# Optimization experiments

Measured on AMD Instinct MI355X. Metric: run time of the kernel, lower is better.

The kernel has to match this reference:

```python
import jax, jax.numpy as jnp
import numpy as np

N, E, D, H = 100000, 200000, 384, 768
BN_EPS = 1e-5


def setup_inputs() -> dict:
    key = jax.random.key(0)
    ks = jax.random.split(key, 8)
    w = lambda k, sh: jax.random.normal(k, sh, jnp.float32) * 0.02
    return {
        "x": jax.random.normal(ks[0], (N, D), jnp.float32),
        "edge_attr": jax.random.normal(ks[1], (E, D), jnp.float32),
        "gamma": jnp.ones((D,), jnp.float32),
        "beta": jnp.zeros((D,), jnp.float32),
        "eps": jnp.zeros((), jnp.float32),          # GINE train_eps, init 0
        "W_edge": w(ks[2], (D, D)),
        "b_edge": jnp.zeros((D,), jnp.float32),
        "W1": w(ks[3], (D, H)),
        "b1": jnp.zeros((H,), jnp.float32),
        "W2": w(ks[4], (H, D)),
        "b2": jnp.zeros((D,), jnp.float32),
        "edge_index": jax.random.randint(ks[5], (2, E), 0, N, jnp.int32),
    }


def reference(x, edge_attr, gamma, beta, eps, W_edge, b_edge, W1, b1, W2, b2, edge_index):
    # BatchNorm1d over the node (batch) dimension, training statistics
    mu = jnp.mean(x, axis=0)
    var = jnp.var(x, axis=0)
    h = (x - mu) * jax.lax.rsqrt(var + BN_EPS) * gamma + beta  # [N, D]

    src, dst = edge_index[0], edge_index[1]  # j -> i (PyG source_to_target)
    # GINEConv message: relu(x_j + lin(edge_attr))
    msg = jax.nn.relu(h[src] + edge_attr @ W_edge + b_edge)     # [E, D]
    agg = jax.ops.segment_sum(msg, dst, num_segments=N)         # sum aggregation

    # nn((1+eps)*x_i + agg) where nn = Linear->GELU->Linear
    z = (1.0 + eps) * h + agg
    z = jax.nn.gelu(z @ W1 + b1, approximate=False) @ W2 + b2

    # residual + outer GELU activation (drop_path/dropout = identity at eval)
    return x + jax.nn.gelu(z, approximate=False)
```

## Files before the change

### kernel.cpp

```cpp
#include <hip/hip_runtime.h>
#include <hip/hip_bf16.h>

#define Df 384
#define Hf 768
#define SCAN_CH 4096

typedef __bf16 bf16x8 __attribute__((ext_vector_type(8)));
typedef float f32x4 __attribute__((ext_vector_type(4)));

struct __attribute__((aligned(4))) U12 { unsigned int x, y, z; };

__device__ inline unsigned short f2bf(float f) {
    __hip_bfloat16 h = __float2bfloat16(f);
    return __builtin_bit_cast(unsigned short, h);
}
__device__ inline float bf2f(unsigned short u) {
    unsigned int v = ((unsigned int)u) << 16;
    return __builtin_bit_cast(float, v);
}
__device__ inline float lobf(unsigned int v) { return bf2f((unsigned short)(v & 0xffff)); }
__device__ inline float hibf(unsigned int v) { return bf2f((unsigned short)(v >> 16)); }
__device__ inline unsigned int pk2(float a, float b) {
    return (unsigned int)f2bf(a) | ((unsigned int)f2bf(b) << 16);
}
__device__ inline float gelu_(float v) {
    return 0.5f * v * (1.0f + erff(v * 0.70710678118654752f));
}
__device__ inline void gload16(const void* g, void* l) {
    __builtin_amdgcn_global_load_lds(
        (const __attribute__((address_space(1))) unsigned int*)g,
        (__attribute__((address_space(3))) unsigned int*)l, 16, 0, 0);
}

__global__ void bn_stats(const float* __restrict__ x, float* __restrict__ stats, int N) {
    int t = threadIdx.x;
    int c4 = (t % 96) * 4;
    int rs = t / 96;
    float s0 = 0, s1 = 0, s2 = 0, s3 = 0, q0 = 0, q1 = 0, q2 = 0, q3 = 0;
    for (int r = blockIdx.x * 2 + rs; r < N; r += gridDim.x * 2) {
        float4 v = *(const float4*)(x + (size_t)r * Df + c4);
        s0 += v.x; s1 += v.y; s2 += v.z; s3 += v.w;
        q0 += v.x * v.x; q1 += v.y * v.y; q2 += v.z * v.z; q3 += v.w * v.w;
    }
    unsafeAtomicAdd(&stats[c4 + 0], s0);
    unsafeAtomicAdd(&stats[c4 + 1], s1);
    unsafeAtomicAdd(&stats[c4 + 2], s2);
    unsafeAtomicAdd(&stats[c4 + 3], s3);
    unsafeAtomicAdd(&stats[Df + c4 + 0], q0);
    unsafeAtomicAdd(&stats[Df + c4 + 1], q1);
    unsafeAtomicAdd(&stats[Df + c4 + 2], q2);
    unsafeAtomicAdd(&stats[Df + c4 + 3], q3);
}

__global__ void bn_finalize(const float* __restrict__ stats,
                            const float* __restrict__ gamma,
                            const float* __restrict__ beta,
                            float* __restrict__ coef, int N) {
    int c = threadIdx.x;
    float invN = 1.0f / (float)N;
    float mu = stats[c] * invN;
    float var = stats[Df + c] * invN - mu * mu;
    float rs = rsqrtf(var + 1e-5f);
    float a = gamma[c] * rs;
    coef[c] = a;
    coef[Df + c] = beta[c] - mu * a;
}

__global__ void h_kernel(const float* __restrict__ x, const float* __restrict__ coef,
                         unsigned short* __restrict__ hb, int tot8) {
    int i = blockIdx.x * 256 + threadIdx.x;
    if (i >= tot8) return;
    size_t base = (size_t)i * 8;
    int c = (int)(base % Df);
    float4 x0 = *(const float4*)(x + base);
    float4 x1 = *(const float4*)(x + base + 4);
    const float* a = coef + c;
    const float* b = coef + Df + c;
    uint4 o;
    o.x = pk2(x0.x * a[0] + b[0], x0.y * a[1] + b[1]);
    o.y = pk2(x0.z * a[2] + b[2], x0.w * a[3] + b[3]);
    o.z = pk2(x1.x * a[4] + b[4], x1.y * a[5] + b[5]);
    o.w = pk2(x1.z * a[6] + b[6], x1.w * a[7] + b[7]);
    *(uint4*)(hb + base) = o;
}

__global__ void wtrans(const float* __restrict__ Wsrc, unsigned short* __restrict__ Wdst,
                       int K, int Nc) {
    int idx = blockIdx.x * 256 + threadIdx.x;
    if (idx >= K * Nc) return;
    int k = idx / Nc, n = idx % Nc;
    Wdst[(size_t)n * K + k] = f2bf(Wsrc[idx]);
}

__global__ void degree_k(const int* __restrict__ dst, int* __restrict__ deg, int E) {
    int e = blockIdx.x * 256 + threadIdx.x;
    if (e < E) atomicAdd(&deg[dst[e]], 1);
}

__global__ void scan1(const int* __restrict__ deg, int* __restrict__ off,
                      int* __restrict__ sums, int N) {
    __shared__ int ts[256];
    int t = threadIdx.x;
    int base = blockIdx.x * SCAN_CH + t * 16;
    int v[16];
    int s = 0;
    for (int j = 0; j < 16; j++) {
        int idx = base + j;
        int d = (idx < N) ? deg[idx] : 0;
        v[j] = s;
        s += d;
    }
    ts[t] = s;
    __syncthreads();
    for (int o = 1; o < 256; o <<= 1) {
        int add = (t >= o) ? ts[t - o] : 0;
        __syncthreads();
        ts[t] += add;
        __syncthreads();
    }
    int pre = t ? ts[t - 1] : 0;
    for (int j = 0; j < 16; j++) {
        int idx = base + j;
        if (idx < N) off[idx] = pre + v[j];
    }
    if (t == 255) sums[blockIdx.x] = ts[255];
}

__global__ void scan2(int* __restrict__ sums, int nb) {
    int acc = 0;
    for (int b = 0; b < nb; b++) { int v = sums[b]; sums[b] = acc; acc += v; }
    sums[nb] = acc;
}

__global__ void scan3(int* __restrict__ off, const int* __restrict__ sums, int N, int nb) {
    int idx = blockIdx.x * 256 + threadIdx.x;
    if (idx < N) off[idx] += sums[idx / SCAN_CH];
    else if (idx == N) off[N] = sums[nb];
}

__global__ void fill_k(const int* __restrict__ dst, const int* __restrict__ src,
                       int* __restrict__ cursor, int* __restrict__ srcp,
                       int* __restrict__ pose, int E) {
    int e = blockIdx.x * 256 + threadIdx.x;
    if (e >= E) return;
    int pos = atomicAdd(&cursor[dst[e]], 1);
    srcp[pos] = src[e];
    pose[e] = pos;
}

__global__ __launch_bounds__(256) void aggregate(
    const unsigned short* __restrict__ msgl, const unsigned short* __restrict__ hb,
    const int* __restrict__ off, const int* __restrict__ srcp,
    const float* __restrict__ epsp,
    unsigned short* __restrict__ zb, int N) {
    int lane = threadIdx.x & 63;
    int wid = threadIdx.x >> 6;
    int nwaves = gridDim.x * 4;
    float s1p = 1.0f + epsp[0];
    int loff = lane * 6;
    for (int i = blockIdx.x * 4 + wid; i < N; i += nwaves) {
        int o0 = off[i], o1 = off[i + 1];
        float a0 = 0, a1 = 0, a2 = 0, a3 = 0, a4 = 0, a5 = 0;
        for (int p = o0; p < o1; ++p) {
            int s = srcp[p];
            U12 mv = *(const U12*)(msgl + (size_t)p * Df + loff);
            U12 hv = *(const U12*)(hb + (size_t)s * Df + loff);
            a0 += fmaxf(lobf(mv.x) + lobf(hv.x), 0.f);
            a1 += fmaxf(hibf(mv.x) + hibf(hv.x), 0.f);
            a2 += fmaxf(lobf(mv.y) + lobf(hv.y), 0.f);
            a3 += fmaxf(hibf(mv.y) + hibf(hv.y), 0.f);
            a4 += fmaxf(lobf(mv.z) + lobf(hv.z), 0.f);
            a5 += fmaxf(hibf(mv.z) + hibf(hv.z), 0.f);
        }
        U12 hv = *(const U12*)(hb + (size_t)i * Df + loff);
        U12 o;
        o.x = pk2(s1p * lobf(hv.x) + a0, s1p * hibf(hv.x) + a1);
        o.y = pk2(s1p * lobf(hv.y) + a2, s1p * hibf(hv.y) + a3);
        o.z = pk2(s1p * lobf(hv.z) + a4, s1p * hibf(hv.z) + a5);
        *(U12*)(zb + (size_t)i * Df + loff) = o;
    }
}

template <int EPI, bool ABF16>
__global__ __launch_bounds__(256) void gemm_fused(
    const void* __restrict__ Ap, const unsigned short* __restrict__ Bt,
    const float* __restrict__ bias, int M, int K,
    const int* __restrict__ pose,
    unsigned short* __restrict__ outb,
    const float* __restrict__ xres, float* __restrict__ outf, int ldo) {
    __shared__ __align__(16) unsigned short As[128 * 32];
    __shared__ __align__(16) unsigned short Bs[128 * 32];
    const int t = threadIdx.x;
    const int n0 = blockIdx.x * 128;
    const int m0 = blockIdx.y * 128;
    const int lane = t & 63;
    const int wid = t >> 6;
    const int wr = (wid >> 1) << 6;
    const int wc = (wid & 1) << 6;
    const int fr = lane & 15;
    const int kg = lane >> 4;
    const int crow = lane >> 2;
    const int cseg = lane & 3;
    const int sr = t >> 1;
    const int sh = (t & 1) << 4;

    f32x4 acc[4][4];
#pragma unroll
    for (int i = 0; i < 4; i++)
#pragma unroll
        for (int j = 0; j < 4; j++) acc[i][j] = (f32x4){0.f, 0.f, 0.f, 0.f};

    const bool arok = (m0 + sr) < M;
    const size_t arowoff = (size_t)(m0 + sr) * K;

    for (int k0 = 0; k0 < K; k0 += 32) {
        if (ABF16) {
            const unsigned short* Ab = (const unsigned short*)Ap;
#pragma unroll
            for (int c = 0; c < 2; c++) {
                const int row = wid * 32 + c * 16 + crow;
                if (m0 + row < M)
                    gload16(Ab + (size_t)(m0 + row) * K + k0 + cseg * 8,
                            &As[(wid * 32 + c * 16) * 32]);
            }
        } else {
            uint4 w0 = {0, 0, 0, 0}, w1 = {0, 0, 0, 0};
            if (arok) {
                const float4* p = (const float4*)((const float*)Ap + arowoff + k0 + sh);
                float4 f0 = p[0], f1 = p[1], f2 = p[2], f3 = p[3];
                w0.x = pk2(f0.x, f0.y); w0.y = pk2(f0.z, f0.w);
                w0.z = pk2(f1.x, f1.y); w0.w = pk2(f1.z, f1.w);
                w1.x = pk2(f2.x, f2.y); w1.y = pk2(f2.z, f2.w);
                w1.z = pk2(f3.x, f3.y); w1.w = pk2(f3.z, f3.w);
            }
            *(uint4*)&As[sr * 32 + sh] = w0;
            *(uint4*)&As[sr * 32 + sh + 8] = w1;
        }
#pragma unroll
        for (int c = 0; c < 2; c++) {
            const int row = wid * 32 + c * 16 + crow;
            gload16(Bt + (size_t)(n0 + row) * K + k0 + cseg * 8,
                    &Bs[(wid * 32 + c * 16) * 32]);
        }
        __syncthreads();
        bf16x8 a[4], b[4];
#pragma unroll
        for (int i = 0; i < 4; i++) a[i] = *(const bf16x8*)&As[(wr + i * 16 + fr) * 32 + kg * 8];
#pragma unroll
        for (int j = 0; j < 4; j++) b[j] = *(const bf16x8*)&Bs[(wc + j * 16 + fr) * 32 + kg * 8];
#pragma unroll
        for (int i = 0; i < 4; i++)
#pragma unroll
            for (int j = 0; j < 4; j++)
                acc[i][j] = __builtin_amdgcn_mfma_f32_16x16x32_bf16(a[i], b[j], acc[i][j], 0, 0, 0);
        __syncthreads();
    }

    const int kg4 = kg * 4;
#pragma unroll
    for (int i = 0; i < 4; i++) {
        const int rb = m0 + wr + i * 16 + kg4;
#pragma unroll
        for (int j = 0; j < 4; j++) {
            const int c = n0 + wc + j * 16 + fr;
#pragma unroll
            for (int r = 0; r < 4; r++) {
                const int row = rb + r;
                if (row < M) {
                    float v = acc[i][j][r] + bias[c];
                    if (EPI == 1) {
                        outb[(size_t)row * ldo + c] = f2bf(gelu_(v));
                    } else if (EPI == 2) {
                        size_t o = (size_t)row * ldo + c;
                        outf[o] = xres[o] + gelu_(v);
                    } else {
                        outb[(size_t)pose[row] * ldo + c] = f2bf(v);
                    }
                }
            }
        }
    }
}

extern "C" void kernel_launch(void* const* d_in, const int* in_sizes, int n_in,
                              void* d_out, int out_size, void* d_ws, size_t ws_size,
                              hipStream_t stream) {
    const float* x = (const float*)d_in[0];
    const float* ea = (const float*)d_in[1];
    const float* gamma = (const float*)d_in[2];
    const float* beta = (const float*)d_in[3];
    const float* epsp = (const float*)d_in[4];
    const float* W_edge = (const float*)d_in[5];
    const float* b_edge = (const float*)d_in[6];
    const float* W1 = (const float*)d_in[7];
    const float* b1 = (const float*)d_in[8];
    const float* W2 = (const float*)d_in[9];
    const float* b2 = (const float*)d_in[10];
    const int* eidx = (const int*)d_in[11];
    float* out = (float*)d_out;
    const int N = in_sizes[0] / Df;
    const int E = in_sizes[1] / Df;
    const int* esrc = eidx;
    const int* edst = eidx + E;

    char* w = (char*)d_ws;
    size_t off_ = 0;
    auto alloc = [&](size_t bytes) { char* p = w + off_; off_ += (bytes + 255) & ~(size_t)255; return p; };
    float* stats = (float*)alloc(2 * Df * sizeof(float));
    float* coef = (float*)alloc(2 * Df * sizeof(float));
    unsigned short* hb = (unsigned short*)alloc((size_t)N * Df * 2);
    unsigned short* zb = (unsigned short*)alloc((size_t)N * Df * 2);
    unsigned short* tb = (unsigned short*)alloc((size_t)N * Hf * 2);
    unsigned short* WeT = (unsigned short*)alloc((size_t)Df * Df * 2);
    unsigned short* W1T = (unsigned short*)alloc((size_t)Df * Hf * 2);
    unsigned short* W2T = (unsigned short*)alloc((size_t)Hf * Df * 2);
    int* deg = (int*)alloc((size_t)(N + 1) * 4);
    int* offs = (int*)alloc((size_t)(N + 1) * 4);
    int* srcp = (int*)alloc((size_t)E * 4);
    int* pose = (int*)alloc((size_t)E * 4);
    int* sums = (int*)alloc(64 * 4);
    size_t msgl_bytes = (size_t)E * Df * 2;
    unsigned short* msgl;
    if (off_ + msgl_bytes <= ws_size) msgl = (unsigned short*)alloc(msgl_bytes);
    else msgl = (unsigned short*)d_out;
    (void)n_in; (void)out_size;

    hipMemsetAsync(stats, 0, 2 * Df * sizeof(float), stream);
    hipMemsetAsync(deg, 0, (size_t)N * 4, stream);

    bn_stats<<<1024, 192, 0, stream>>>(x, stats, N);
    bn_finalize<<<1, Df, 0, stream>>>(stats, gamma, beta, coef, N);
    int tot8 = N * Df / 8;
    h_kernel<<<(tot8 + 255) / 256, 256, 0, stream>>>(x, coef, hb, tot8);

    wtrans<<<(Df * Df + 255) / 256, 256, 0, stream>>>(W_edge, WeT, Df, Df);
    wtrans<<<(Df * Hf + 255) / 256, 256, 0, stream>>>(W1, W1T, Df, Hf);
    wtrans<<<(Hf * Df + 255) / 256, 256, 0, stream>>>(W2, W2T, Hf, Df);

    int nb = (N + SCAN_CH - 1) / SCAN_CH;
    degree_k<<<(E + 255) / 256, 256, 0, stream>>>(edst, deg, E);
    scan1<<<nb, 256, 0, stream>>>(deg, offs, sums, N);
    scan2<<<1, 1, 0, stream>>>(sums, nb);
    scan3<<<(N + 256) / 256, 256, 0, stream>>>(offs, sums, N, nb);
    hipMemcpyAsync(deg, offs, (size_t)N * 4, hipMemcpyDeviceToDevice, stream);
    fill_k<<<(E + 255) / 256, 256, 0, stream>>>(edst, esrc, deg, srcp, pose, E);

    dim3 ge(Df / 128, (E + 127) / 128);
    gemm_fused<3, false><<<ge, 256, 0, stream>>>(ea, WeT, b_edge, E, Df,
                                                 pose, msgl, nullptr, nullptr, Df);

    aggregate<<<2048, 256, 0, stream>>>(msgl, hb, offs, srcp, epsp, zb, N);

    dim3 g1(Hf / 128, (N + 127) / 128);
    gemm_fused<1, true><<<g1, 256, 0, stream>>>(zb, W1T, b1, N, Df,
                                                nullptr, tb, nullptr, nullptr, Hf);
    dim3 g2(Df / 128, (N + 127) / 128);
    gemm_fused<2, true><<<g2, 256, 0, stream>>>(tb, W2T, b2, N, Hf,
                                                nullptr, nullptr, x, out, Df);
}
```

Before: 1.114 ms.

## Double-buffer GEMM LDS tiles and remap workgroups across XCDs

The GEMM kernel now double-buffers its A and B shared-memory tiles, so the global loads for the next K tile are issued before the MFMAs on the current tile. This removes one barrier per iteration and lets memory latency overlap with compute. Launches switch to a 1D grid whose block ids are remapped so consecutive tiles, which share A rows, land on the same XCD for better L2 reuse. The cost is twice the LDS per block, which may lower occupancy, plus more registers held across the loop for the fp32 A prefetch.

```diff
diff --git a/kernel.cpp b/kernel.cpp
--- a/kernel.cpp
+++ b/kernel.cpp
@@ -184,15 +184,22 @@
 template <int EPI, bool ABF16>
 __global__ __launch_bounds__(256) void gemm_fused(
     const void* __restrict__ Ap, const unsigned short* __restrict__ Bt,
-    const float* __restrict__ bias, int M, int K,
+    const float* __restrict__ bias, int M, int K, int ncols,
     const int* __restrict__ pose,
     unsigned short* __restrict__ outb,
     const float* __restrict__ xres, float* __restrict__ outf, int ldo) {
-    __shared__ __align__(16) unsigned short As[128 * 32];
-    __shared__ __align__(16) unsigned short Bs[128 * 32];
+    __shared__ __align__(16) unsigned short As[2][128 * 32];
+    __shared__ __align__(16) unsigned short Bs[2][128 * 32];
     const int t = threadIdx.x;
-    const int n0 = blockIdx.x * 128;
-    const int m0 = blockIdx.y * 128;
+    const int nwg = gridDim.x;
+    const int orig = blockIdx.x;
+    const int xcd = orig & 7;
+    const int q = nwg >> 3, r = nwg & 7;
+    const int wgid = (xcd < r ? xcd * (q + 1) : r * (q + 1) + (xcd - r) * q) + (orig >> 3);
+    const int pp = wgid / ncols;
+    const int m0 = pp * 128;
+    const int n0 = (wgid - pp * ncols) * 128;
+
     const int lane = t & 63;
     const int wid = t >> 6;
     const int wr = (wid >> 1) << 6;
@@ -212,48 +219,81 @@
 
     const bool arok = (m0 + sr) < M;
     const size_t arowoff = (size_t)(m0 + sr) * K;
-
-    for (int k0 = 0; k0 < K; k0 += 32) {
-        if (ABF16) {
-            const unsigned short* Ab = (const unsigned short*)Ap;
-#pragma unroll
-            for (int c = 0; c < 2; c++) {
-                const int row = wid * 32 + c * 16 + crow;
-                if (m0 + row < M)
-                    gload16(Ab + (size_t)(m0 + row) * K + k0 + cseg * 8,
-                            &As[(wid * 32 + c * 16) * 32]);
+    const int NT = K >> 5;
+
+    auto stageB = [&](int buf, int k0) {
+#pragma unroll
+        for (int h = 0; h < 2; h++) {
+            const int rbase = wid * 32 + h * 16;
+            gload16(Bt + (size_t)(n0 + rbase + crow) * K + k0 + cseg * 8,
+                    &Bs[buf][rbase * 32]);
+        }
+    };
+    auto stageA16 = [&](int buf, int k0) {
+        const unsigned short* Ab = (const unsigned short*)Ap;
+#pragma unroll
+        for (int h = 0; h < 2; h++) {
+            const int rbase = wid * 32 + h * 16;
+            if (m0 + rbase + crow < M)
+                gload16(Ab + (size_t)(m0 + rbase + crow) * K + k0 + cseg * 8,
+                        &As[buf][rbase * 32]);
+        }
+    };
+
+    if (ABF16) {
+        stageA16(0, 0);
+    } else if (arok) {
+        const float4* p = (const float4*)((const float*)Ap + arowoff + sh);
+        float4 f0 = p[0], f1 = p[1], f2 = p[2], f3 = p[3];
+        uint4 w0, w1;
+        w0.x = pk2(f0.x, f0.y); w0.y = pk2(f0.z, f0.w);
+        w0.z = pk2(f1.x, f1.y); w0.w = pk2(f1.z, f1.w);
+        w1.x = pk2(f2.x, f2.y); w1.y = pk2(f2.z, f2.w);
+        w1.z = pk2(f3.x, f3.y); w1.w = pk2(f3.z, f3.w);
+        *(uint4*)&As[0][sr * 32 + sh] = w0;
+        *(uint4*)&As[0][sr * 32 + sh + 8] = w1;
+    }
+    stageB(0, 0);
+    __syncthreads();
+
+    int cur = 0;
+    for (int kt = 0; kt < NT; ++kt) {
+        const int nxt = cur ^ 1;
+        const bool more = (kt + 1) < NT;
+        float4 f0, f1, f2, f3;
+        if (more) {
+            const int k0n = (kt + 1) * 32;
+            if (ABF16) {
+                stageA16(nxt, k0n);
+            } else if (arok) {
+                const float4* p = (const float4*)((const float*)Ap + arowoff + k0n + sh);
+                f0 = p[0]; f1 = p[1]; f2 = p[2]; f3 = p[3];
             }
-        } else {
-            uint4 w0 = {0, 0, 0, 0}, w1 = {0, 0, 0, 0};
-            if (arok) {
-                const float4* p = (const float4*)((const float*)Ap + arowoff + k0 + sh);
-                float4 f0 = p[0], f1 = p[1], f2 = p[2], f3 = p[3];
-                w0.x = pk2(f0.x, f0.y); w0.y = pk2(f0.z, f0.w);
-                w0.z = pk2(f1.x, f1.y); w0.w = pk2(f1.z, f1.w);
-                w1.x = pk2(f2.x, f2.y); w1.y = pk2(f2.z, f2.w);
-                w1.z = pk2(f3.x, f3.y); w1.w = pk2(f3.z, f3.w);
-            }
-            *(uint4*)&As[sr * 32 + sh] = w0;
-            *(uint4*)&As[sr * 32 + sh + 8] = w1;
-        }
-#pragma unroll
-        for (int c = 0; c < 2; c++) {
-            const int row = wid * 32 + c * 16 + crow;
-            gload16(Bt + (size_t)(n0 + row) * K + k0 + cseg * 8,
-                    &Bs[(wid * 32 + c * 16) * 32]);
-        }
-        __syncthreads();
+            stageB(nxt, k0n);
+        }
+
         bf16x8 a[4], b[4];
 #pragma unroll
-        for (int i = 0; i < 4; i++) a[i] = *(const bf16x8*)&As[(wr + i * 16 + fr) * 32 + kg * 8];
-#pragma unroll
-        for (int j = 0; j < 4; j++) b[j] = *(const bf16x8*)&Bs[(wc + j * 16 + fr) * 32 + kg * 8];
+        for (int i = 0; i < 4; i++) a[i] = *(const bf16x8*)&As[cur][(wr + i * 16 + fr) * 32 + kg * 8];
+#pragma unroll
+        for (int j = 0; j < 4; j++) b[j] = *(const bf16x8*)&Bs[cur][(wc + j * 16 + fr) * 32 + kg * 8];
 #pragma unroll
         for (int i = 0; i < 4; i++)
 #pragma unroll
             for (int j = 0; j < 4; j++)
                 acc[i][j] = __builtin_amdgcn_mfma_f32_16x16x32_bf16(a[i], b[j], acc[i][j], 0, 0, 0);
+
+        if (!ABF16 && more && arok) {
+            uint4 w0, w1;
+            w0.x = pk2(f0.x, f0.y); w0.y = pk2(f0.z, f0.w);
+            w0.z = pk2(f1.x, f1.y); w0.w = pk2(f1.z, f1.w);
+            w1.x = pk2(f2.x, f2.y); w1.y = pk2(f2.z, f2.w);
+            w1.z = pk2(f3.x, f3.y); w1.w = pk2(f3.z, f3.w);
+            *(uint4*)&As[nxt][sr * 32 + sh] = w0;
+            *(uint4*)&As[nxt][sr * 32 + sh + 8] = w1;
+        }
         __syncthreads();
+        cur = nxt;
     }
 
     const int kg4 = kg * 4;
@@ -345,16 +385,15 @@
     hipMemcpyAsync(deg, offs, (size_t)N * 4, hipMemcpyDeviceToDevice, stream);
     fill_k<<<(E + 255) / 256, 256, 0, stream>>>(edst, esrc, deg, srcp, pose, E);
 
-    dim3 ge(Df / 128, (E + 127) / 128);
-    gemm_fused<3, false><<<ge, 256, 0, stream>>>(ea, WeT, b_edge, E, Df,
-                                                 pose, msgl, nullptr, nullptr, Df);
+    int ep = (E + 127) / 128;
+    gemm_fused<3, false><<<dim3(ep * (Df / 128)), 256, 0, stream>>>(
+        ea, WeT, b_edge, E, Df, Df / 128, pose, msgl, nullptr, nullptr, Df);
 
     aggregate<<<2048, 256, 0, stream>>>(msgl, hb, offs, srcp, epsp, zb, N);
 
-    dim3 g1(Hf / 128, (N + 127) / 128);
-    gemm_fused<1, true><<<g1, 256, 0, stream>>>(zb, W1T, b1, N, Df,
-                                                nullptr, tb, nullptr, nullptr, Hf);
-    dim3 g2(Df / 128, (N + 127) / 128);
-    gemm_fused<2, true><<<g2, 256, 0, stream>>>(tb, W2T, b2, N, Hf,
-                                                nullptr, nullptr, x, out, Df);
-}
+    int np = (N + 127) / 128;
+    gemm_fused<1, true><<<dim3(np * (Hf / 128)), 256, 0, stream>>>(
+        zb, W1T, b1, N, Df, Hf / 128, nullptr, tb, nullptr, nullptr, Hf);
+    gemm_fused<2, true><<<dim3(np * (Df / 128)), 256, 0, stream>>>(
+        tb, W2T, b2, N, Hf, Df / 128, nullptr, nullptr, x, out, Df);
+}
```

New measurement: 1.085 ms. -2.6%, faster.

## Restructure GEMMs with 256x64 tiles, register-prefetched A and chunk-staged B

Applied to the files above, without the earlier changes.

Replaces the 128x128 LDS-tiled GEMM with a 256x64 tile kernel. Each wave streams its A rows straight from global memory into registers with a multi-stage prefetch, while B (the weights) is staged into LDS in large K chunks with an XOR swizzle. This cuts per-K-step barriers and LDS traffic for A. Workgroup IDs are remapped across XCDs for cache locality, and launch bounds request 3 waves per SIMD. The costs are higher register pressure and uncoalesced direct global reads for A fragments.

```diff
diff --git a/kernel.cpp b/kernel.cpp
--- a/kernel.cpp
+++ b/kernel.cpp
@@ -181,28 +181,38 @@
     }
 }
 
-template <int EPI, bool ABF16>
-__global__ __launch_bounds__(256) void gemm_fused(
+template <int NTK, int EPI, bool ABF16>
+__global__ __launch_bounds__(256, 3) void gemm2(
     const void* __restrict__ Ap, const unsigned short* __restrict__ Bt,
-    const float* __restrict__ bias, int M, int K,
+    const float* __restrict__ bias, int M, int ncols,
     const int* __restrict__ pose,
     unsigned short* __restrict__ outb,
     const float* __restrict__ xres, float* __restrict__ outf, int ldo) {
-    __shared__ __align__(16) unsigned short As[128 * 32];
-    __shared__ __align__(16) unsigned short Bs[128 * 32];
+    constexpr int K = NTK * 32;
+    constexpr int NCH = (NTK + 11) / 12;
+    constexpr int CKT = NTK / NCH;
+    constexpr int D = ABF16 ? 3 : 2;
+    constexpr int PW = ABF16 ? 4 : 8;
+    __shared__ __align__(16) unsigned short Bs[CKT * 64 * 32];
+
     const int t = threadIdx.x;
-    const int n0 = blockIdx.x * 128;
-    const int m0 = blockIdx.y * 128;
+    const int nwg = gridDim.x;
+    const int orig = blockIdx.x;
+    const int xcd = orig & 7;
+    const int q = nwg >> 3, r = nwg & 7;
+    const int wgid = (xcd < r ? xcd * (q + 1) : r * (q + 1) + (xcd - r) * q) + (orig >> 3);
+    const int pp = wgid / ncols;
+    const int m0 = pp * 256;
+    const int n0 = (wgid - pp * ncols) * 64;
+
     const int lane = t & 63;
     const int wid = t >> 6;
-    const int wr = (wid >> 1) << 6;
-    const int wc = (wid & 1) << 6;
     const int fr = lane & 15;
     const int kg = lane >> 4;
     const int crow = lane >> 2;
     const int cseg = lane & 3;
-    const int sr = t >> 1;
-    const int sh = (t & 1) << 4;
+    const int ssw = (crow >> 1) & 3;
+    const int bseg = kg ^ ((fr >> 1) & 3);
 
     f32x4 acc[4][4];
 #pragma unroll
@@ -210,64 +220,104 @@
 #pragma unroll
         for (int j = 0; j < 4; j++) acc[i][j] = (f32x4){0.f, 0.f, 0.f, 0.f};
 
-    const bool arok = (m0 + sr) < M;
-    const size_t arowoff = (size_t)(m0 + sr) * K;
-
-    for (int k0 = 0; k0 < K; k0 += 32) {
-        if (ABF16) {
-            const unsigned short* Ab = (const unsigned short*)Ap;
-#pragma unroll
-            for (int c = 0; c < 2; c++) {
-                const int row = wid * 32 + c * 16 + crow;
-                if (m0 + row < M)
-                    gload16(Ab + (size_t)(m0 + row) * K + k0 + cseg * 8,
-                            &As[(wid * 32 + c * 16) * 32]);
+    int arow[4];
+#pragma unroll
+    for (int i = 0; i < 4; i++) {
+        int rr = m0 + wid * 64 + i * 16 + fr;
+        arow[i] = rr < M ? rr : M - 1;
+    }
+
+    auto stageB = [&](int ch) {
+        const int ktw = wid * 3;
+#pragma unroll
+        for (int c = 0; c < 3; c++) {
+#pragma unroll
+            for (int rb = 0; rb < 64; rb += 16) {
+                const int col = n0 + rb + crow;
+                const int kk = (ch * CKT + ktw + c) * 32 + ((cseg ^ ssw) << 3);
+                gload16(Bt + (size_t)col * K + kk,
+                        &Bs[((ktw + c) * 64 + rb) * 32]);
             }
-        } else {
-            uint4 w0 = {0, 0, 0, 0}, w1 = {0, 0, 0, 0};
-            if (arok) {
-                const float4* p = (const float4*)((const float*)Ap + arowoff + k0 + sh);
-                float4 f0 = p[0], f1 = p[1], f2 = p[2], f3 = p[3];
-                w0.x = pk2(f0.x, f0.y); w0.y = pk2(f0.z, f0.w);
-                w0.z = pk2(f1.x, f1.y); w0.w = pk2(f1.z, f1.w);
-                w1.x = pk2(f2.x, f2.y); w1.y = pk2(f2.z, f2.w);
-                w1.z = pk2(f3.x, f3.y); w1.w = pk2(f3.z, f3.w);
+        }
+    };
+    auto issueA = [&](int kt, uint4* dst) {
+#pragma unroll
+        for (int i = 0; i < 4; i++) {
+            if (ABF16) {
+                dst[i] = *(const uint4*)((const unsigned short*)Ap +
+                                         (size_t)arow[i] * K + kt * 32 + kg * 8);
+            } else {
+                const float* p = (const float*)Ap + (size_t)arow[i] * K + kt * 32 + kg * 8;
+                dst[2 * i] = *(const uint4*)p;
+                dst[2 * i + 1] = *(const uint4*)(p + 4);
             }
-            *(uint4*)&As[sr * 32 + sh] = w0;
-            *(uint4*)&As[sr * 32 + sh + 8] = w1;
-        }
-#pragma unroll
-        for (int c = 0; c < 2; c++) {
-            const int row = wid * 32 + c * 16 + crow;
-            gload16(Bt + (size_t)(n0 + row) * K + k0 + cseg * 8,
-                    &Bs[(wid * 32 + c * 16) * 32]);
-        }
-        __syncthreads();
-        bf16x8 a[4], b[4];
-#pragma unroll
-        for (int i = 0; i < 4; i++) a[i] = *(const bf16x8*)&As[(wr + i * 16 + fr) * 32 + kg * 8];
-#pragma unroll
-        for (int j = 0; j < 4; j++) b[j] = *(const bf16x8*)&Bs[(wc + j * 16 + fr) * 32 + kg * 8];
-#pragma unroll
-        for (int i = 0; i < 4; i++)
+        }
+    };
+    auto toFrag = [&](const uint4* src, bf16x8* a) {
+#pragma unroll
+        for (int i = 0; i < 4; i++) {
+            if (ABF16) {
+                a[i] = __builtin_bit_cast(bf16x8, src[i]);
+            } else {
+                float4 x0 = __builtin_bit_cast(float4, src[2 * i]);
+                float4 x1 = __builtin_bit_cast(float4, src[2 * i + 1]);
+                uint4 u;
+                u.x = pk2(x0.x, x0.y); u.y = pk2(x0.z, x0.w);
+                u.z = pk2(x1.x, x1.y); u.w = pk2(x1.z, x1.w);
+                a[i] = __builtin_bit_cast(bf16x8, u);
+            }
+        }
+    };
+
+    uint4 pf[D][PW];
+    stageB(0);
+#pragma unroll
+    for (int d = 0; d < D; d++)
+        issueA(d < NTK ? d : NTK - 1, pf[d]);
+    __syncthreads();
+
+#pragma unroll
+    for (int ch = 0; ch < NCH; ch++) {
+        if (ch > 0) {
+            __syncthreads();
+            stageB(ch);
+            __syncthreads();
+        }
+#pragma unroll
+        for (int k = 0; k < CKT; k++) {
+            const int kt = ch * CKT + k;
+            bf16x8 b[4];
 #pragma unroll
             for (int j = 0; j < 4; j++)
-                acc[i][j] = __builtin_amdgcn_mfma_f32_16x16x32_bf16(a[i], b[j], acc[i][j], 0, 0, 0);
-        __syncthreads();
-    }
+                b[j] = *(const bf16x8*)((const char*)Bs +
+                                        ((k * 64 + j * 16 + fr) * 64 + bseg * 16));
+            bf16x8 a[4];
+            toFrag(pf[kt % D], a);
+            if (kt + D < NTK) issueA(kt + D, pf[(kt + D) % D]);
+#pragma unroll
+            for (int i = 0; i < 4; i++)
+#pragma unroll
+                for (int j = 0; j < 4; j++)
+                    acc[i][j] = __builtin_amdgcn_mfma_f32_16x16x32_bf16(a[i], b[j], acc[i][j], 0, 0, 0);
+        }
+    }
+
+    float bi[4];
+#pragma unroll
+    for (int j = 0; j < 4; j++) bi[j] = bias[n0 + j * 16 + fr];
 
     const int kg4 = kg * 4;
 #pragma unroll
     for (int i = 0; i < 4; i++) {
-        const int rb = m0 + wr + i * 16 + kg4;
+        const int rb = m0 + wid * 64 + i * 16 + kg4;
 #pragma unroll
         for (int j = 0; j < 4; j++) {
-            const int c = n0 + wc + j * 16 + fr;
+            const int c = n0 + j * 16 + fr;
 #pragma unroll
             for (int r = 0; r < 4; r++) {
                 const int row = rb + r;
                 if (row < M) {
-                    float v = acc[i][j][r] + bias[c];
+                    float v = acc[i][j][r] + bi[j];
                     if (EPI == 1) {
                         outb[(size_t)row * ldo + c] = f2bf(gelu_(v));
                     } else if (EPI == 2) {
@@ -345,16 +395,15 @@
     hipMemcpyAsync(deg, offs, (size_t)N * 4, hipMemcpyDeviceToDevice, stream);
     fill_k<<<(E + 255) / 256, 256, 0, stream>>>(edst, esrc, deg, srcp, pose, E);
 
-    dim3 ge(Df / 128, (E + 127) / 128);
-    gemm_fused<3, false><<<ge, 256, 0, stream>>>(ea, WeT, b_edge, E, Df,
-                                                 pose, msgl, nullptr, nullptr, Df);
+    int ep2 = (E + 255) / 256;
+    gemm2<12, 3, false><<<dim3(ep2 * (Df / 64)), 256, 0, stream>>>(
+        ea, WeT, b_edge, E, Df / 64, pose, msgl, nullptr, nullptr, Df);
 
     aggregate<<<2048, 256, 0, stream>>>(msgl, hb, offs, srcp, epsp, zb, N);
 
-    dim3 g1(Hf / 128, (N + 127) / 128);
-    gemm_fused<1, true><<<g1, 256, 0, stream>>>(zb, W1T, b1, N, Df,
-                                                nullptr, tb, nullptr, nullptr, Hf);
-    dim3 g2(Df / 128, (N + 127) / 128);
-    gemm_fused<2, true><<<g2, 256, 0, stream>>>(tb, W2T, b2, N, Hf,
-                                                nullptr, nullptr, x, out, Df);
-}
+    int np2 = (N + 255) / 256;
+    gemm2<12, 1, true><<<dim3(np2 * (Hf / 64)), 256, 0, stream>>>(
+        zb, W1T, b1, N, Hf / 64, nullptr, tb, nullptr, nullptr, Hf);
+    gemm2<24, 2, true><<<dim3(np2 * (Df / 64)), 256, 0, stream>>>(
+        tb, W2T, b2, N, Df / 64, nullptr, nullptr, x, out, Df);
+}
```

After: 1.214 ms. 1.09x slower.

## Replace GEMMs with 256x128 triple-buffered swizzled-LDS kernel and pre-cast edge_attr

Applied to the files above, without the earlier changes.

Replaces the 128x128 single-buffered GEMM with a 512-thread kernel using 256x128 tiles, K-step 64, a triple-buffered LDS ring filled by async global-to-LDS loads, XOR-swizzled LDS layout, vmcnt-based waits instead of full syncthreads, s_setprio around MFMA bursts, and XCD-aware workgroup remapping. Edge attributes are now cast to bf16 by a separate kernel into the tb buffer so all three GEMMs take bf16 A operands. This aims to overlap memory loads with MFMA work and cut LDS bank conflicts and barrier stalls. The cost is an extra fp32-to-bf16 pass over edge_attr, larger LDS use per block, and reliance on a fixed count of outstanding loads for correctness.

```diff
diff --git a/kernel.cpp b/kernel.cpp
--- a/kernel.cpp
+++ b/kernel.cpp
@@ -82,6 +82,18 @@
     o.z = pk2(x1.x * a[4] + b[4], x1.y * a[5] + b[5]);
     o.w = pk2(x1.z * a[6] + b[6], x1.w * a[7] + b[7]);
     *(uint4*)(hb + base) = o;
+}
+
+__global__ void cast_bf16(const float* __restrict__ src, unsigned short* __restrict__ dst, int tot8) {
+    int i = blockIdx.x * 256 + threadIdx.x;
+    if (i >= tot8) return;
+    size_t base = (size_t)i * 8;
+    float4 x0 = *(const float4*)(src + base);
+    float4 x1 = *(const float4*)(src + base + 4);
+    uint4 o;
+    o.x = pk2(x0.x, x0.y); o.y = pk2(x0.z, x0.w);
+    o.z = pk2(x1.x, x1.y); o.w = pk2(x1.z, x1.w);
+    *(uint4*)(dst + base) = o;
 }
 
 __global__ void wtrans(const float* __restrict__ Wsrc, unsigned short* __restrict__ Wdst,
@@ -181,28 +193,35 @@
     }
 }
 
-template <int EPI, bool ABF16>
-__global__ __launch_bounds__(256) void gemm_fused(
-    const void* __restrict__ Ap, const unsigned short* __restrict__ Bt,
-    const float* __restrict__ bias, int M, int K,
+template <int NT, int EPI>
+__global__ __launch_bounds__(512, 1) void gemm8(
+    const unsigned short* __restrict__ Ab, const unsigned short* __restrict__ Bt,
+    const float* __restrict__ bias, int M, int ncols,
     const int* __restrict__ pose,
     unsigned short* __restrict__ outb,
     const float* __restrict__ xres, float* __restrict__ outf, int ldo) {
-    __shared__ __align__(16) unsigned short As[128 * 32];
-    __shared__ __align__(16) unsigned short Bs[128 * 32];
+    constexpr int K = NT * 64;
+    __shared__ __align__(16) unsigned short As[3 * 256 * 64];
+    __shared__ __align__(16) unsigned short Bs[3 * 128 * 64];
+
     const int t = threadIdx.x;
-    const int n0 = blockIdx.x * 128;
-    const int m0 = blockIdx.y * 128;
+    const int nwg = gridDim.x;
+    const int orig = blockIdx.x;
+    const int xcd = orig & 7;
+    const int q = nwg >> 3, r = nwg & 7;
+    const int wgid = (xcd < r ? xcd * (q + 1) : r * (q + 1) + (xcd - r) * q) + (orig >> 3);
+    const int pp = wgid / ncols;
+    const int m0 = pp * 256;
+    const int n0 = (wgid - pp * ncols) * 128;
+
     const int lane = t & 63;
     const int wid = t >> 6;
-    const int wr = (wid >> 1) << 6;
-    const int wc = (wid & 1) << 6;
     const int fr = lane & 15;
     const int kg = lane >> 4;
-    const int crow = lane >> 2;
-    const int cseg = lane & 3;
-    const int sr = t >> 1;
-    const int sh = (t & 1) << 4;
+    const int wm = wid >> 1;
+    const int wn = wid & 1;
+    const int srow = lane >> 3;
+    const int scol = (lane & 7) ^ srow;
 
     f32x4 acc[4][4];
 #pragma unroll
@@ -210,64 +229,101 @@
 #pragma unroll
         for (int j = 0; j < 4; j++) acc[i][j] = (f32x4){0.f, 0.f, 0.f, 0.f};
 
-    const bool arok = (m0 + sr) < M;
-    const size_t arowoff = (size_t)(m0 + sr) * K;
-
-    for (int k0 = 0; k0 < K; k0 += 32) {
-        if (ABF16) {
-            const unsigned short* Ab = (const unsigned short*)Ap;
-#pragma unroll
-            for (int c = 0; c < 2; c++) {
-                const int row = wid * 32 + c * 16 + crow;
-                if (m0 + row < M)
-                    gload16(Ab + (size_t)(m0 + row) * K + k0 + cseg * 8,
-                            &As[(wid * 32 + c * 16) * 32]);
-            }
-        } else {
-            uint4 w0 = {0, 0, 0, 0}, w1 = {0, 0, 0, 0};
-            if (arok) {
-                const float4* p = (const float4*)((const float*)Ap + arowoff + k0 + sh);
-                float4 f0 = p[0], f1 = p[1], f2 = p[2], f3 = p[3];
-                w0.x = pk2(f0.x, f0.y); w0.y = pk2(f0.z, f0.w);
-                w0.z = pk2(f1.x, f1.y); w0.w = pk2(f1.z, f1.w);
-                w1.x = pk2(f2.x, f2.y); w1.y = pk2(f2.z, f2.w);
-                w1.z = pk2(f3.x, f3.y); w1.w = pk2(f3.z, f3.w);
-            }
-            *(uint4*)&As[sr * 32 + sh] = w0;
-            *(uint4*)&As[sr * 32 + sh + 8] = w1;
-        }
-#pragma unroll
-        for (int c = 0; c < 2; c++) {
-            const int row = wid * 32 + c * 16 + crow;
-            gload16(Bt + (size_t)(n0 + row) * K + k0 + cseg * 8,
-                    &Bs[(wid * 32 + c * 16) * 32]);
-        }
-        __syncthreads();
+#define STG_A(u, kt_, bufi) do {                                                \
+        int rr_ = m0 + (u) * 64 + wid * 8 + srow;                               \
+        if (rr_ >= M) rr_ = M - 1;                                              \
+        gload16(Ab + (size_t)rr_ * K + (kt_) * 64 + (scol << 3),                \
+                &As[(bufi) * 16384 + (u) * 4096 + wid * 512]);                  \
+    } while (0)
+#define STG_B(u, kt_, bufi) do {                                                \
+        int rr_ = n0 + (u) * 64 + wid * 8 + srow;                               \
+        gload16(Bt + (size_t)rr_ * K + (kt_) * 64 + (scol << 3),                \
+                &Bs[(bufi) * 8192 + (u) * 4096 + wid * 512]);                   \
+    } while (0)
+
+#pragma unroll
+    for (int u = 0; u < 4; u++) STG_A(u, 0, 0);
+    STG_B(0, 0, 0); STG_B(1, 0, 0);
+#pragma unroll
+    for (int u = 0; u < 4; u++) STG_A(u, 1, 1);
+    STG_B(0, 1, 1); STG_B(1, 1, 1);
+    asm volatile("s_waitcnt vmcnt(6)" ::: "memory");
+    __builtin_amdgcn_s_barrier();
+    asm volatile("" ::: "memory");
+
+    for (int kt = 0; kt < NT; ++kt) {
+        const unsigned short* Ac = As + (kt % 3) * 16384;
+        const unsigned short* Bc = Bs + (kt % 3) * 8192;
+        const int nb = (kt + 2) % 3;
+        const bool st = (kt + 2) < NT;
+
+        if (st) { STG_A(0, kt + 2, nb); STG_A(1, kt + 2, nb); }
+
         bf16x8 a[4], b[4];
 #pragma unroll
-        for (int i = 0; i < 4; i++) a[i] = *(const bf16x8*)&As[(wr + i * 16 + fr) * 32 + kg * 8];
-#pragma unroll
-        for (int j = 0; j < 4; j++) b[j] = *(const bf16x8*)&Bs[(wc + j * 16 + fr) * 32 + kg * 8];
+        for (int i = 0; i < 4; i++) {
+            const int row = wm * 64 + i * 16 + fr;
+            a[i] = *(const bf16x8*)&Ac[row * 64 + ((kg ^ (row & 7)) << 3)];
+        }
+#pragma unroll
+        for (int j = 0; j < 4; j++) {
+            const int row = wn * 64 + j * 16 + fr;
+            b[j] = *(const bf16x8*)&Bc[row * 64 + ((kg ^ (row & 7)) << 3)];
+        }
+        if (st) { STG_A(2, kt + 2, nb); STG_A(3, kt + 2, nb); }
+        __builtin_amdgcn_s_setprio(1);
 #pragma unroll
         for (int i = 0; i < 4; i++)
 #pragma unroll
             for (int j = 0; j < 4; j++)
                 acc[i][j] = __builtin_amdgcn_mfma_f32_16x16x32_bf16(a[i], b[j], acc[i][j], 0, 0, 0);
-        __syncthreads();
-    }
+        __builtin_amdgcn_s_setprio(0);
+
+        if (st) { STG_B(0, kt + 2, nb); STG_B(1, kt + 2, nb); }
+#pragma unroll
+        for (int i = 0; i < 4; i++) {
+            const int row = wm * 64 + i * 16 + fr;
+            a[i] = *(const bf16x8*)&Ac[row * 64 + (((4 + kg) ^ (row & 7)) << 3)];
+        }
+#pragma unroll
+        for (int j = 0; j < 4; j++) {
+            const int row = wn * 64 + j * 16 + fr;
+            b[j] = *(const bf16x8*)&Bc[row * 64 + (((4 + kg) ^ (row & 7)) << 3)];
+        }
+        __builtin_amdgcn_s_setprio(1);
+#pragma unroll
+        for (int i = 0; i < 4; i++)
+#pragma unroll
+            for (int j = 0; j < 4; j++)
+                acc[i][j] = __builtin_amdgcn_mfma_f32_16x16x32_bf16(a[i], b[j], acc[i][j], 0, 0, 0);
+        __builtin_amdgcn_s_setprio(0);
+
+        if (kt < NT - 1) {
+            if (st) asm volatile("s_waitcnt vmcnt(6)" ::: "memory");
+            else    asm volatile("s_waitcnt vmcnt(0)" ::: "memory");
+            __builtin_amdgcn_s_barrier();
+            asm volatile("" ::: "memory");
+        }
+    }
+#undef STG_A
+#undef STG_B
+
+    float bi[4];
+#pragma unroll
+    for (int j = 0; j < 4; j++) bi[j] = bias[n0 + wn * 64 + j * 16 + fr];
 
     const int kg4 = kg * 4;
 #pragma unroll
     for (int i = 0; i < 4; i++) {
-        const int rb = m0 + wr + i * 16 + kg4;
+        const int rb = m0 + wm * 64 + i * 16 + kg4;
 #pragma unroll
         for (int j = 0; j < 4; j++) {
-            const int c = n0 + wc + j * 16 + fr;
+            const int c = n0 + wn * 64 + j * 16 + fr;
 #pragma unroll
             for (int r = 0; r < 4; r++) {
                 const int row = rb + r;
                 if (row < M) {
-                    float v = acc[i][j][r] + bias[c];
+                    float v = acc[i][j][r] + bi[j];
                     if (EPI == 1) {
                         outb[(size_t)row * ldo + c] = f2bf(gelu_(v));
                     } else if (EPI == 2) {
@@ -323,6 +379,7 @@
     unsigned short* msgl;
     if (off_ + msgl_bytes <= ws_size) msgl = (unsigned short*)alloc(msgl_bytes);
     else msgl = (unsigned short*)d_out;
+    unsigned short* eab = tb;
     (void)n_in; (void)out_size;
 
     hipMemsetAsync(stats, 0, 2 * Df * sizeof(float), stream);
@@ -332,6 +389,9 @@
     bn_finalize<<<1, Df, 0, stream>>>(stats, gamma, beta, coef, N);
     int tot8 = N * Df / 8;
     h_kernel<<<(tot8 + 255) / 256, 256, 0, stream>>>(x, coef, hb, tot8);
+
+    int etot8 = E * Df / 8;
+    cast_bf16<<<(etot8 + 255) / 256, 256, 0, stream>>>(ea, eab, etot8);
 
     wtrans<<<(Df * Df + 255) / 256, 256, 0, stream>>>(W_edge, WeT, Df, Df);
     wtrans<<<(Df * Hf + 255) / 256, 256, 0, stream>>>(W1, W1T, Df, Hf);
@@ -345,16 +405,15 @@
     hipMemcpyAsync(deg, offs, (size_t)N * 4, hipMemcpyDeviceToDevice, stream);
     fill_k<<<(E + 255) / 256, 256, 0, stream>>>(edst, esrc, deg, srcp, pose, E);
 
-    dim3 ge(Df / 128, (E + 127) / 128);
-    gemm_fused<3, false><<<ge, 256, 0, stream>>>(ea, WeT, b_edge, E, Df,
-                                                 pose, msgl, nullptr, nullptr, Df);
+    int ep = (E + 255) / 256;
+    gemm8<6, 3><<<dim3(ep * (Df / 128)), 512, 0, stream>>>(
+        eab, WeT, b_edge, E, Df / 128, pose, msgl, nullptr, nullptr, Df);
 
     aggregate<<<2048, 256, 0, stream>>>(msgl, hb, offs, srcp, epsp, zb, N);
 
-    dim3 g1(Hf / 128, (N + 127) / 128);
-    gemm_fused<1, true><<<g1, 256, 0, stream>>>(zb, W1T, b1, N, Df,
-                                                nullptr, tb, nullptr, nullptr, Hf);
-    dim3 g2(Df / 128, (N + 127) / 128);
-    gemm_fused<2, true><<<g2, 256, 0, stream>>>(tb, W2T, b2, N, Hf,
-                                                nullptr, nullptr, x, out, Df);
-}
+    int np = (N + 255) / 256;
+    gemm8<6, 1><<<dim3(np * (Hf / 128)), 512, 0, stream>>>(
+        zb, W1T, b1, N, Hf / 128, nullptr, tb, nullptr, nullptr, Hf);
+    gemm8<12, 2><<<dim3(np * (Df / 128)), 512, 0, stream>>>(
+        tb, W2T, b2, N, Df / 128, nullptr, nullptr, x, out, Df);
+}
```

After: 1.121 ms. Within noise of the previous version (+0.7%).
